# Optimization experiments

Hardware: AMD Instinct MI355X
Metric: run time of the kernel (lower is better)

## Reference

```python
import jax, jax.numpy as jnp
import numpy as np

MARGIN = 10.0
EPS = 1e-8


def setup_inputs() -> dict:
    key = jax.random.key(0)
    k1, k2, k3 = jax.random.split(key, 3)
    V, B, C, D = 2, 16384, 100, 512
    feat = jax.random.normal(k1, (V, B, D), dtype=jnp.float32)
    label = jax.random.randint(k2, (B,), 0, C, dtype=jnp.int64)
    anchor = jax.random.normal(k3, (V, C, D), dtype=jnp.float32)
    return {"feat": feat, "label": label, "anchor": anchor}


def reference(feat, label, anchor):
    # feat: [V, B, D], label: [B], anchor: [V, C, D]
    V, B, D = feat.shape
    C = anchor.shape[1]

    # ----- per-view center loss + cosine similarity -----
    centers = anchor[:, label, :]                      # [V, B, D] gather
    diff = feat - centers
    center_loss = jnp.sum(diff * diff, axis=(1, 2)) / 2.0 / B   # [V]

    fn = jnp.maximum(jnp.linalg.norm(feat, axis=-1), EPS)        # [V, B]
    cn = jnp.maximum(jnp.linalg.norm(centers, axis=-1), EPS)     # [V, B]
    sims = jnp.sum(feat * centers, axis=-1) / (fn * cn)          # [V, B]

    # ----- inter-class margin loss (vectorized pairwise sq-dist) -----
    sq = jnp.sum(anchor * anchor, axis=-1)             # [V, C]
    gram = jnp.einsum('vcd,ved->vce', anchor, anchor)  # [V, C, C]
    pd = sq[:, :, None] + sq[:, None, :] - 2.0 * gram  # [V, C, C] squared dists
    # sum over i<j = (full sum - diagonal) / 2; diagonal is 0 analytically
    diag = jnp.einsum('vcc->v', pd)
    pair_sum = (jnp.sum(pd, axis=(1, 2)) - diag) * 0.5            # [V]
    inter = pair_sum / (C * (C - 1))
    inter_loss = jnp.maximum(MARGIN - inter, 0.0)                 # [V]

    loss = jnp.mean(center_loss) + jnp.mean(inter_loss)
    return loss, sims
```

## Files before the change

### kernel.cpp

```cpp
#include <hip/hip_runtime.h>
#include <math.h>

namespace {
constexpr int V = 2;
constexpr int B = 16384;
constexpr int C = 100;
constexpr int D = 512;
constexpr float MARGIN = 10.0f;
constexpr float EPS = 1e-8f;
constexpr int ROWS_PER_BLOCK = 4;
constexpr int NBLOCKS = (V * B) / ROWS_PER_BLOCK;
}

__global__ __launch_bounds__(256) void row_kernel(
    const float* __restrict__ feat, const int* __restrict__ label,
    const float* __restrict__ anchor, float* __restrict__ sims,
    float* __restrict__ partials)
{
    const int wave = threadIdx.x >> 6;
    const int lane = threadIdx.x & 63;
    const int row  = blockIdx.x * ROWS_PER_BLOCK + wave;
    const int v = row >> 14;
    const int b = row & (B - 1);
    const float* frow = feat + (size_t)row * D;
    const float* crow = anchor + ((size_t)v * C + label[b]) * D;

    float s_ff = 0.f, s_cc = 0.f, s_fc = 0.f, s_dd = 0.f;
#pragma unroll
    for (int h = 0; h < 2; ++h) {
        const int d = h * 256 + lane * 4;
        const float4 f = *reinterpret_cast<const float4*>(frow + d);
        const float4 c = *reinterpret_cast<const float4*>(crow + d);
        s_ff += f.x*f.x + f.y*f.y + f.z*f.z + f.w*f.w;
        s_cc += c.x*c.x + c.y*c.y + c.z*c.z + c.w*c.w;
        s_fc += f.x*c.x + f.y*c.y + f.z*c.z + f.w*c.w;
        const float dx = f.x-c.x, dy = f.y-c.y, dz = f.z-c.z, dw = f.w-c.w;
        s_dd += dx*dx + dy*dy + dz*dz + dw*dw;
    }
#pragma unroll
    for (int off = 32; off; off >>= 1) {
        s_ff += __shfl_xor(s_ff, off);
        s_cc += __shfl_xor(s_cc, off);
        s_fc += __shfl_xor(s_fc, off);
        s_dd += __shfl_xor(s_dd, off);
    }
    __shared__ float blk[ROWS_PER_BLOCK];
    if (lane == 0) {
        const float fn = fmaxf(sqrtf(s_ff), EPS);
        const float cn = fmaxf(sqrtf(s_cc), EPS);
        sims[row] = s_fc / (fn * cn);
        blk[wave] = s_dd;
    }
    __syncthreads();
    if (threadIdx.x == 0)
        partials[blockIdx.x] = blk[0] + blk[1] + blk[2] + blk[3];
}

__global__ __launch_bounds__(512) void inter_kernel(
    const float* __restrict__ anchor, float* __restrict__ inter_out)
{
    const int v = blockIdx.x;
    const int d = threadIdx.x;
    const float* a = anchor + (size_t)v * C * D;
    float m = 0.f, s = 0.f;
#pragma unroll 4
    for (int c = 0; c < C; ++c) {
        const float x = a[(size_t)c * D + d];
        m += x;
        s += x * x;
    }
    float mm = m * m;
#pragma unroll
    for (int off = 32; off; off >>= 1) {
        s  += __shfl_xor(s, off);
        mm += __shfl_xor(mm, off);
    }
    __shared__ float rs[8], rm[8];
    const int wave = threadIdx.x >> 6, lane = threadIdx.x & 63;
    if (lane == 0) { rs[wave] = s; rm[wave] = mm; }
    __syncthreads();
    if (threadIdx.x == 0) {
        float S = 0.f, MM = 0.f;
        for (int w = 0; w < 8; ++w) { S += rs[w]; MM += rm[w]; }
        const float inter = ((float)C * S - MM) / (float)(C * (C - 1));
        inter_out[v] = fmaxf(MARGIN - inter, 0.f);
    }
}

__global__ __launch_bounds__(1024) void finalize_kernel(
    const float* __restrict__ partials, const float* __restrict__ inter,
    float* __restrict__ out)
{
    const int vv = threadIdx.x >> 9;
    const int t  = threadIdx.x & 511;
    float s = 0.f;
#pragma unroll
    for (int i = 0; i < 8; ++i)
        s += partials[vv * (NBLOCKS / 2) + t + i * 512];
    const int wave = threadIdx.x >> 6, lane = threadIdx.x & 63;
#pragma unroll
    for (int off = 32; off; off >>= 1) s += __shfl_xor(s, off);
    __shared__ float red[16];
    if (lane == 0) red[wave] = s;
    __syncthreads();
    if (threadIdx.x == 0) {
        float cl0 = 0.f, cl1 = 0.f;
        for (int w = 0; w < 8;  ++w) cl0 += red[w];
        for (int w = 8; w < 16; ++w) cl1 += red[w];
        const float center_mean = (cl0 + cl1) / (4.0f * (float)B);
        const float inter_mean  = 0.5f * (inter[0] + inter[1]);
        out[0] = center_mean + inter_mean;
    }
}

extern "C" void kernel_launch(void* const* d_in, const int* in_sizes, int n_in,
                              void* d_out, int out_size, void* d_ws, size_t ws_size,
                              hipStream_t stream)
{
    const float* feat   = (const float*)d_in[0];
    const int*   label  = (const int*)d_in[1];
    const float* anchor = (const float*)d_in[2];
    float* out      = (float*)d_out;
    float* ws       = (float*)d_ws;
    float* partials = ws;
    float* inter    = ws + NBLOCKS;
    float* sims     = out + 1;

    hipLaunchKernelGGL(inter_kernel, dim3(V), dim3(512), 0, stream,
                       anchor, inter);
    hipLaunchKernelGGL(row_kernel, dim3(NBLOCKS), dim3(256), 0, stream,
                       feat, label, anchor, sims, partials);
    hipLaunchKernelGGL(finalize_kernel, dim3(1), dim3(1024), 0, stream,
                       partials, inter, out);
}
```

Baseline: 108.2 us.

## Fuse inter-class reduction into row kernel and process four rows per wave

Merges the separate two-block inter-class kernel into the main row kernel as 16 extra blocks that each reduce a chunk of anchor classes and write partial column sums, which are then combined in finalize. Each wave now handles four rows and accumulates the squared-difference sum across them, which cuts the block count from 8192 to 2048 and shrinks the partials array. This removes one kernel launch and the serial, poorly parallel inter kernel. In exchange, finalize does more work and each wave carries a longer dependency chain.

```diff
diff --git a/kernel.cpp b/kernel.cpp
--- a/kernel.cpp
+++ b/kernel.cpp
@@ -8,108 +8,128 @@
 constexpr int D = 512;
 constexpr float MARGIN = 10.0f;
 constexpr float EPS = 1e-8f;
-constexpr int ROWS_PER_BLOCK = 4;
-constexpr int NBLOCKS = (V * B) / ROWS_PER_BLOCK;
+
+constexpr int RB = 2048;
+constexpr int ROWS_PER_WAVE = 4;
+constexpr int IB_PER_V = 8;
+constexpr int IB = V * IB_PER_V;
+constexpr int CHUNK = 13;
 }
 
-__global__ __launch_bounds__(256) void row_kernel(
+__global__ __launch_bounds__(256) void main_kernel(
     const float* __restrict__ feat, const int* __restrict__ label,
     const float* __restrict__ anchor, float* __restrict__ sims,
-    float* __restrict__ partials)
+    float* __restrict__ ws)
 {
+    __shared__ float blk[4];
     const int wave = threadIdx.x >> 6;
     const int lane = threadIdx.x & 63;
-    const int row  = blockIdx.x * ROWS_PER_BLOCK + wave;
-    const int v = row >> 14;
-    const int b = row & (B - 1);
-    const float* frow = feat + (size_t)row * D;
-    const float* crow = anchor + ((size_t)v * C + label[b]) * D;
 
-    float s_ff = 0.f, s_cc = 0.f, s_fc = 0.f, s_dd = 0.f;
+    if (blockIdx.x < RB) {
+        const int wid = blockIdx.x * 4 + wave;
+        float s_dd = 0.f;
 #pragma unroll
-    for (int h = 0; h < 2; ++h) {
-        const int d = h * 256 + lane * 4;
-        const float4 f = *reinterpret_cast<const float4*>(frow + d);
-        const float4 c = *reinterpret_cast<const float4*>(crow + d);
-        s_ff += f.x*f.x + f.y*f.y + f.z*f.z + f.w*f.w;
-        s_cc += c.x*c.x + c.y*c.y + c.z*c.z + c.w*c.w;
-        s_fc += f.x*c.x + f.y*c.y + f.z*c.z + f.w*c.w;
-        const float dx = f.x-c.x, dy = f.y-c.y, dz = f.z-c.z, dw = f.w-c.w;
-        s_dd += dx*dx + dy*dy + dz*dz + dw*dw;
-    }
+        for (int r = 0; r < ROWS_PER_WAVE; ++r) {
+            const int row = wid * ROWS_PER_WAVE + r;
+            const int v = row >> 14;
+            const int b = row & (B - 1);
+            const float* frow = feat + (size_t)row * D;
+            const float* crow = anchor + ((size_t)v * C + label[b]) * D;
+            float s_ff = 0.f, s_cc = 0.f, s_fc = 0.f;
 #pragma unroll
-    for (int off = 32; off; off >>= 1) {
-        s_ff += __shfl_xor(s_ff, off);
-        s_cc += __shfl_xor(s_cc, off);
-        s_fc += __shfl_xor(s_fc, off);
-        s_dd += __shfl_xor(s_dd, off);
-    }
-    __shared__ float blk[ROWS_PER_BLOCK];
-    if (lane == 0) {
-        const float fn = fmaxf(sqrtf(s_ff), EPS);
-        const float cn = fmaxf(sqrtf(s_cc), EPS);
-        sims[row] = s_fc / (fn * cn);
-        blk[wave] = s_dd;
-    }
-    __syncthreads();
-    if (threadIdx.x == 0)
-        partials[blockIdx.x] = blk[0] + blk[1] + blk[2] + blk[3];
-}
-
-__global__ __launch_bounds__(512) void inter_kernel(
-    const float* __restrict__ anchor, float* __restrict__ inter_out)
-{
-    const int v = blockIdx.x;
-    const int d = threadIdx.x;
-    const float* a = anchor + (size_t)v * C * D;
-    float m = 0.f, s = 0.f;
-#pragma unroll 4
-    for (int c = 0; c < C; ++c) {
-        const float x = a[(size_t)c * D + d];
-        m += x;
-        s += x * x;
-    }
-    float mm = m * m;
+            for (int h = 0; h < 2; ++h) {
+                const int d = h * 256 + lane * 4;
+                const float4 f = *reinterpret_cast<const float4*>(frow + d);
+                const float4 c = *reinterpret_cast<const float4*>(crow + d);
+                s_ff += f.x*f.x + f.y*f.y + f.z*f.z + f.w*f.w;
+                s_cc += c.x*c.x + c.y*c.y + c.z*c.z + c.w*c.w;
+                s_fc += f.x*c.x + f.y*c.y + f.z*c.z + f.w*c.w;
+                const float dx = f.x-c.x, dy = f.y-c.y, dz = f.z-c.z, dw = f.w-c.w;
+                s_dd += dx*dx + dy*dy + dz*dz + dw*dw;
+            }
 #pragma unroll
-    for (int off = 32; off; off >>= 1) {
-        s  += __shfl_xor(s, off);
-        mm += __shfl_xor(mm, off);
-    }
-    __shared__ float rs[8], rm[8];
-    const int wave = threadIdx.x >> 6, lane = threadIdx.x & 63;
-    if (lane == 0) { rs[wave] = s; rm[wave] = mm; }
-    __syncthreads();
-    if (threadIdx.x == 0) {
-        float S = 0.f, MM = 0.f;
-        for (int w = 0; w < 8; ++w) { S += rs[w]; MM += rm[w]; }
-        const float inter = ((float)C * S - MM) / (float)(C * (C - 1));
-        inter_out[v] = fmaxf(MARGIN - inter, 0.f);
+            for (int off = 32; off; off >>= 1) {
+                s_ff += __shfl_xor(s_ff, off);
+                s_cc += __shfl_xor(s_cc, off);
+                s_fc += __shfl_xor(s_fc, off);
+            }
+            if (lane == 0) {
+                const float fn = fmaxf(sqrtf(s_ff), EPS);
+                const float cn = fmaxf(sqrtf(s_cc), EPS);
+                sims[row] = s_fc / (fn * cn);
+            }
+        }
+#pragma unroll
+        for (int off = 32; off; off >>= 1) s_dd += __shfl_xor(s_dd, off);
+        if (lane == 0) blk[wave] = s_dd;
+        __syncthreads();
+        if (threadIdx.x == 0)
+            ws[blockIdx.x] = blk[0] + blk[1] + blk[2] + blk[3];
+    } else {
+        const int ib = blockIdx.x - RB;
+        const int v = ib >> 3, chunk = ib & 7;
+        const int c0 = chunk * CHUNK;
+        const int c1 = (c0 + CHUNK < C) ? c0 + CHUNK : C;
+        const float* a = anchor + (size_t)v * C * D;
+        const int d0 = threadIdx.x, d1 = threadIdx.x + 256;
+        float m0 = 0.f, m1 = 0.f, s = 0.f;
+        for (int c = c0; c < c1; ++c) {
+            const float x0 = a[(size_t)c * D + d0];
+            const float x1 = a[(size_t)c * D + d1];
+            m0 += x0; m1 += x1; s += x0*x0 + x1*x1;
+        }
+        float* im = ws + RB + IB;
+        im[ib * D + d0] = m0;
+        im[ib * D + d1] = m1;
+#pragma unroll
+        for (int off = 32; off; off >>= 1) s += __shfl_xor(s, off);
+        if (lane == 0) blk[wave] = s;
+        __syncthreads();
+        if (threadIdx.x == 0)
+            ws[RB + ib] = blk[0] + blk[1] + blk[2] + blk[3];
     }
 }
 
 __global__ __launch_bounds__(1024) void finalize_kernel(
-    const float* __restrict__ partials, const float* __restrict__ inter,
-    float* __restrict__ out)
+    const float* __restrict__ ws, float* __restrict__ out)
 {
-    const int vv = threadIdx.x >> 9;
-    const int t  = threadIdx.x & 511;
-    float s = 0.f;
+    const float* partials = ws;
+    const float* is = ws + RB;
+    const float* im = ws + RB + IB;
+    const int t = threadIdx.x;
+    const int wave = t >> 6, lane = t & 63;
+
+    float sdd = partials[t] + partials[t + 1024];
+
+    const int v = t >> 9, d = t & 511;
+    float m = 0.f;
 #pragma unroll
-    for (int i = 0; i < 8; ++i)
-        s += partials[vv * (NBLOCKS / 2) + t + i * 512];
-    const int wave = threadIdx.x >> 6, lane = threadIdx.x & 63;
+    for (int k = 0; k < IB_PER_V; ++k)
+        m += im[((size_t)v * IB_PER_V + k) * D + d];
+    float mm = m * m;
+
 #pragma unroll
-    for (int off = 32; off; off >>= 1) s += __shfl_xor(s, off);
-    __shared__ float red[16];
-    if (lane == 0) red[wave] = s;
+    for (int off = 32; off; off >>= 1) {
+        sdd += __shfl_xor(sdd, off);
+        mm  += __shfl_xor(mm, off);
+    }
+    __shared__ float rdd[16], rmm[16];
+    if (lane == 0) { rdd[wave] = sdd; rmm[wave] = mm; }
     __syncthreads();
-    if (threadIdx.x == 0) {
-        float cl0 = 0.f, cl1 = 0.f;
-        for (int w = 0; w < 8;  ++w) cl0 += red[w];
-        for (int w = 8; w < 16; ++w) cl1 += red[w];
-        const float center_mean = (cl0 + cl1) / (4.0f * (float)B);
-        const float inter_mean  = 0.5f * (inter[0] + inter[1]);
-        out[0] = center_mean + inter_mean;
+    if (t == 0) {
+        float ddt = 0.f;
+        for (int w = 0; w < 16; ++w) ddt += rdd[w];
+        float MM0 = 0.f, MM1 = 0.f;
+        for (int w = 0; w < 8;  ++w) MM0 += rmm[w];
+        for (int w = 8; w < 16; ++w) MM1 += rmm[w];
+        float S0 = 0.f, S1 = 0.f;
+        for (int k = 0; k < IB_PER_V; ++k) { S0 += is[k]; S1 += is[IB_PER_V + k]; }
+        const float denom = (float)(C * (C - 1));
+        const float inter0 = ((float)C * S0 - MM0) / denom;
+        const float inter1 = ((float)C * S1 - MM1) / denom;
+        const float il = 0.5f * (fmaxf(MARGIN - inter0, 0.f) +
+                                 fmaxf(MARGIN - inter1, 0.f));
+        out[0] = ddt / (4.0f * (float)B) + il;
     }
 }
 
@@ -120,16 +140,12 @@
     const float* feat   = (const float*)d_in[0];
     const int*   label  = (const int*)d_in[1];
     const float* anchor = (const float*)d_in[2];
-    float* out      = (float*)d_out;
-    float* ws       = (float*)d_ws;
-    float* partials = ws;
-    float* inter    = ws + NBLOCKS;
-    float* sims     = out + 1;
+    float* out  = (float*)d_out;
+    float* ws   = (float*)d_ws;
+    float* sims = out + 1;
 
-    hipLaunchKernelGGL(inter_kernel, dim3(V), dim3(512), 0, stream,
-                       anchor, inter);
-    hipLaunchKernelGGL(row_kernel, dim3(NBLOCKS), dim3(256), 0, stream,
-                       feat, label, anchor, sims, partials);
+    hipLaunchKernelGGL(main_kernel, dim3(RB + IB), dim3(256), 0, stream,
+                       feat, label, anchor, sims, ws);
     hipLaunchKernelGGL(finalize_kernel, dim3(1), dim3(1024), 0, stream,
-                       partials, inter, out);
+                       ws, out);
 }
```

Measured after the change: 98.35 us. -9.1%, faster.
